# Kernel optimization log

Measured on AMD Instinct MI355X. Metric: run time of the kernel, lower is better.

## Reference

```python
import jax, jax.numpy as jnp
import numpy as np

FG_THRESH = 0.5

def _descriptors(fmap, scribbles):
    # fmap: [B, C, h, w]; scribbles: [B, I, H, W]
    B, C, h, w = fmap.shape
    I = scribbles.shape[1]
    # bilinear resize (align_corners=False == half-pixel, no antialias, like torch)
    sr = jax.image.resize(scribbles, (B, I, h, w), method='bilinear', antialias=False)
    mask = (sr > FG_THRESH).astype(fmap.dtype)                 # [B, I, h, w]
    cnt = mask.sum(axis=(-1, -2))                              # [B, I]
    ssum = jnp.einsum('bihw,bchw->bic', mask, fmap)            # masked sum over HW
    mean = ssum / jnp.maximum(cnt, 1.0)[..., None]             # [B, I, C]
    # fallback when a mask has no foreground pixels: feature at argmax of soft mask
    idx = jnp.argmax(sr.reshape(B, I, h * w), axis=-1)         # [B, I]
    fflat = fmap.reshape(B, C, h * w)
    fb = jnp.take_along_axis(fflat, idx[:, None, :], axis=2)   # [B, C, I]
    fb = fb.transpose(0, 2, 1)                                 # [B, I, C]
    return jnp.where((cnt > 0)[..., None], mean, fb)

def setup_inputs() -> dict:
    key = jax.random.key(0)
    k0, k1, k2, k3 = jax.random.split(key, 4)
    return {
        'feat0': jax.random.normal(k0, (8, 256, 128, 128), dtype=jnp.float32),
        'feat1': jax.random.normal(k1, (8, 256, 64, 64), dtype=jnp.float32),
        'feat2': jax.random.normal(k2, (8, 256, 32, 32), dtype=jnp.float32),
        'scribbles': jax.random.uniform(k3, (8, 16, 512, 512), dtype=jnp.float32),
    }

def reference(feat0, feat1, feat2, scribbles):
    # multi_scale=True, random_bg_queries=False: per-level masked mean pool,
    # then average descriptors across feature levels. Output: [B, I, C]
    d0 = _descriptors(feat0, scribbles)
    d1 = _descriptors(feat1, scribbles)
    d2 = _descriptors(feat2, scribbles)
    return (d0 + d1 + d2) / 3.0
```

## Files before the change

kernel.cpp:

```cpp
#include <hip/hip_runtime.h>
#include <stdint.h>

#define NB 8
#define NI 16
#define NC 256
#define SH 512
#define NCH 84

typedef __bf16 bf16x8 __attribute__((ext_vector_type(8)));
typedef float f32x4 __attribute__((ext_vector_type(4)));
typedef uint32_t u32x4 __attribute__((ext_vector_type(4)));

static const size_t OFF_SSUM = 0;
static const size_t OFF_CNT  = OFF_SSUM + (size_t)3 * NB * NI * NC * 4;
static const size_t OFF_KEY  = OFF_CNT + (size_t)3 * NB * NI * 4;
static const size_t WS_NEED  = OFF_KEY + (size_t)3 * NB * NI * 8;
static const int    ZERO_N4  = (int)(WS_NEED / 16);

__device__ __forceinline__ float4 ld4(const float* p) {
    return *reinterpret_cast<const float4*>(p);
}

__global__ __launch_bounds__(256) void zero_kernel(float4* __restrict__ ws4) {
    const int i = blockIdx.x * 256 + threadIdx.x;
    if (i < ZERO_N4) ws4[i] = make_float4(0.f, 0.f, 0.f, 0.f);
}

__device__ __forceinline__ void mfma_step1(const uint16_t* __restrict__ lmp, int ks, int cl,
                                           const float4 (&buf)[2], f32x4& a0) {
    const uint4 wA = *reinterpret_cast<const uint4*>(lmp + ks * 32);
    u32x4 au;
    au.x = ((wA.x >> cl) & 0x10001u) * 0x3F80u;
    au.y = ((wA.y >> cl) & 0x10001u) * 0x3F80u;
    au.z = ((wA.z >> cl) & 0x10001u) * 0x3F80u;
    au.w = ((wA.w >> cl) & 0x10001u) * 0x3F80u;
    const bf16x8 av = __builtin_bit_cast(bf16x8, au);
    bf16x8 bv;
    bv[0] = (__bf16)buf[0].x; bv[1] = (__bf16)buf[0].y;
    bv[2] = (__bf16)buf[0].z; bv[3] = (__bf16)buf[0].w;
    bv[4] = (__bf16)buf[1].x; bv[5] = (__bf16)buf[1].y;
    bv[6] = (__bf16)buf[1].z; bv[7] = (__bf16)buf[1].w;
    a0 = __builtin_amdgcn_mfma_f32_16x16x32_bf16(av, bv, a0, 0, 0, 0);
}

template<int W, int S, int P>
__device__ __forceinline__ void do_chunk(const float* __restrict__ f,
                                         const float* __restrict__ scr,
                                         float* __restrict__ ssum_lb,
                                         int* __restrict__ cnt_lb,
                                         unsigned long long* __restrict__ key_lb,
                                         int b, int chunk, int tid,
                                         uint8_t* __restrict__ lmask8,
                                         uint16_t* __restrict__ lmask16,
                                         int* __restrict__ lcnt,
                                         unsigned long long* __restrict__ lkey) {
    const int wave = tid >> 6;
    const int lane = tid & 63;
    const int kg = lane >> 4;
    const int cl = lane & 15;
    const int c0 = wave * 16;
    const int kb = chunk * 256;
    const float* fp0 = f + ((size_t)b * NC + c0 + cl) * P + kb + kg * 8;
    float4 buf[4][2];
    #pragma unroll
    for (int k = 0; k < 2; ++k) {
        buf[k][0] = ld4(fp0 + k * 32);
        buf[k][1] = ld4(fp0 + k * 32 + 4);
    }

    const int gi = tid >> 8;
    const int p = tid & 255;
    const int pix = chunk * 256 + p;
    const int y = pix / W;
    const int x = pix - y * W;
    const int r0 = S * y + (S / 2 - 1);
    const int c0s = S * x + (S / 2 - 1);
    const float* sb = scr + ((size_t)b * NI + gi * 4) * (SH * SH) + (size_t)r0 * SH;
    float s4v[4];
    if constexpr (S == 4) {
        float4 q0[4], q1[4];
        #pragma unroll
        for (int i = 0; i < 4; ++i) {
            const float* sp = sb + (size_t)i * (SH * SH);
            q0[i] = ld4(sp + (c0s - 1));
            q1[i] = ld4(sp + SH + (c0s - 1));
        }
        #pragma unroll
        for (int i = 0; i < 4; ++i)
            s4v[i] = (q0[i].y + q0[i].z) + (q1[i].y + q1[i].z);
    } else {
        float qa[4], qb[4], qc[4], qd[4];
        #pragma unroll
        for (int i = 0; i < 4; ++i) {
            const float* sp = sb + (size_t)i * (SH * SH);
            qa[i] = sp[c0s];
            qb[i] = sp[c0s + 1];
            qc[i] = sp[SH + c0s];
            qd[i] = sp[SH + c0s + 1];
        }
        #pragma unroll
        for (int i = 0; i < 4; ++i)
            s4v[i] = (qa[i] + qb[i]) + (qc[i] + qd[i]);
    }
    unsigned int mword = 0;
    #pragma unroll
    for (int i = 0; i < 4; ++i) {
        const float s4 = s4v[i];
        bool bit = s4 > 2.0f;
        mword |= bit ? (1u << i) : 0u;
        unsigned long long bal = __ballot(bit);
        if (lane == 0) atomicAdd(&lcnt[gi * 4 + i], (int)__popcll(bal));
        if (bal == 0ull) {
            unsigned int srb = __float_as_uint(0.25f * s4);
            unsigned int mx = srb;
            #pragma unroll
            for (int off = 1; off < 64; off <<= 1) {
                unsigned int o = __shfl_xor(mx, off, 64);
                mx = (o > mx) ? o : mx;
            }
            unsigned long long win = __ballot(srb == mx);
            if (lane == 0) {
                int wl = __ffsll((unsigned long long)win) - 1;
                unsigned int wpix = (unsigned int)(chunk * 256 + (p & ~63) + wl);
                unsigned long long key = (((unsigned long long)mx) << 32)
                                       | (unsigned long long)(0xFFFFFFFFu - wpix);
                atomicMax(&lkey[gi * 4 + i], key);
            }
        }
    }
    lmask8[gi * 256 + p] = (uint8_t)mword;
    __syncthreads();
    if (tid < 256)
        lmask16[tid] = (uint16_t)((unsigned)lmask8[tid]
                                | ((unsigned)lmask8[256 + tid] << 4)
                                | ((unsigned)lmask8[512 + tid] << 8)
                                | ((unsigned)lmask8[768 + tid] << 12));
    __syncthreads();

    #pragma unroll
    for (int k = 2; k < 4; ++k) {
        buf[k][0] = ld4(fp0 + k * 32);
        buf[k][1] = ld4(fp0 + k * 32 + 4);
    }
    const uint16_t* lmp = lmask16 + kg * 8;
    f32x4 acc = {0.f, 0.f, 0.f, 0.f};
    #pragma unroll
    for (int ks = 0; ks < 8; ++ks) {
        mfma_step1(lmp, ks, cl, buf[ks & 3], acc);
        if (ks + 4 < 8) {
            buf[ks & 3][0] = ld4(fp0 + (ks + 4) * 32);
            buf[ks & 3][1] = ld4(fp0 + (ks + 4) * 32 + 4);
        }
    }
    const int c = c0 + cl;
    #pragma unroll
    for (int r = 0; r < 4; ++r)
        atomicAdd(&ssum_lb[(kg * 4 + r) * NC + c], acc[r]);

    if (tid < NI) {
        int v = lcnt[tid];
        if (v) atomicAdd(&cnt_lb[tid], v);
        unsigned long long k = lkey[tid];
        if (k) atomicMax(&key_lb[tid], k);
    }
}

__global__ __launch_bounds__(1024, 8) void fused_kernel(const float* __restrict__ f0,
                                                        const float* __restrict__ f1,
                                                        const float* __restrict__ f2,
                                                        const float* __restrict__ scr,
                                                        float* __restrict__ ssum,
                                                        int* __restrict__ cnt,
                                                        unsigned long long* __restrict__ key) {
    __shared__ uint8_t lmask8[1024];
    __shared__ __align__(16) uint16_t lmask16[256];
    __shared__ int lcnt[NI];
    __shared__ unsigned long long lkey[NI];
    const int tid = threadIdx.x;
    const int b = blockIdx.y;
    const int bx = blockIdx.x;
    if (tid < NI) { lcnt[tid] = 0; lkey[tid] = 0ull; }
    __syncthreads();
    if (bx < 64) {
        const size_t o = (size_t)(0 * NB + b);
        do_chunk<128, 4, 16384>(f0, scr, ssum + o * NI * NC, cnt + o * NI, key + o * NI,
                                b, bx, tid, lmask8, lmask16, lcnt, lkey);
    } else if (bx < 80) {
        const size_t o = (size_t)(1 * NB + b);
        do_chunk<64, 8, 4096>(f1, scr, ssum + o * NI * NC, cnt + o * NI, key + o * NI,
                              b, bx - 64, tid, lmask8, lmask16, lcnt, lkey);
    } else {
        const size_t o = (size_t)(2 * NB + b);
        do_chunk<32, 16, 1024>(f2, scr, ssum + o * NI * NC, cnt + o * NI, key + o * NI,
                               b, bx - 80, tid, lmask8, lmask16, lcnt, lkey);
    }
}

__global__ __launch_bounds__(256) void final_kernel(const float* __restrict__ f0,
                                                    const float* __restrict__ f1,
                                                    const float* __restrict__ f2,
                                                    const int* __restrict__ cnt,
                                                    const unsigned long long* __restrict__ key,
                                                    const float* __restrict__ ssum,
                                                    float* __restrict__ out) {
    const int bi = blockIdx.x;
    const int c = threadIdx.x;
    const int b = bi >> 4;
    const float* fl[3] = {f0, f1, f2};
    const int Ps[3] = {16384, 4096, 1024};
    float r = 0.f;
    #pragma unroll
    for (int l = 0; l < 3; ++l) {
        const int cn = cnt[l * NB * NI + bi];
        float v;
        if (cn > 0) {
            v = ssum[((size_t)l * NB * NI + bi) * NC + c] / (float)cn;
        } else {
            unsigned int p = 0xFFFFFFFFu -
                (unsigned int)(key[l * NB * NI + bi] & 0xFFFFFFFFull);
            v = fl[l][((size_t)b * NC + c) * Ps[l] + p];
        }
        r += v;
    }
    out[(size_t)bi * NC + c] = r * (1.f / 3.f);
}

extern "C" void kernel_launch(void* const* d_in, const int* in_sizes, int n_in,
                              void* d_out, int out_size, void* d_ws, size_t ws_size,
                              hipStream_t stream) {
    const float* f0  = (const float*)d_in[0];
    const float* f1  = (const float*)d_in[1];
    const float* f2  = (const float*)d_in[2];
    const float* scr = (const float*)d_in[3];
    float* out = (float*)d_out;
    char* ws = (char*)d_ws;
    if (ws_size < WS_NEED) return;

    float* ssum = (float*)(ws + OFF_SSUM);
    int* cnt = (int*)(ws + OFF_CNT);
    unsigned long long* key = (unsigned long long*)(ws + OFF_KEY);

    zero_kernel<<<(ZERO_N4 + 255) / 256, 256, 0, stream>>>((float4*)ws);
    fused_kernel<<<dim3(NCH, NB), 1024, 0, stream>>>(f0, f1, f2, scr, ssum, cnt, key);
    final_kernel<<<NB * NI, NC, 0, stream>>>(f0, f1, f2, cnt, key, ssum, out);
}
```

Baseline: 61.61 us.

## Stage feature tiles through swizzled LDS with coalesced loads for MFMA

Features are now loaded with fully coalesced float4 reads into a 64KB XOR-swizzled shared-memory buffer, one 64-channel slab at a time, instead of each lane reading strided rows directly. The MFMA loop reads its B operand from LDS, and each wave covers a K-half across four channel slabs, so there are four accumulators. The next slab is prefetched into registers while the current one is consumed. Scribble loads are split into two halves to reduce register pressure. The 64KB LDS and the extra barriers per slab limit occupancy and add sync overhead.

```diff
diff --git a/kernel.cpp b/kernel.cpp
--- a/kernel.cpp
+++ b/kernel.cpp
@@ -24,23 +24,6 @@
 __global__ __launch_bounds__(256) void zero_kernel(float4* __restrict__ ws4) {
     const int i = blockIdx.x * 256 + threadIdx.x;
     if (i < ZERO_N4) ws4[i] = make_float4(0.f, 0.f, 0.f, 0.f);
-}
-
-__device__ __forceinline__ void mfma_step1(const uint16_t* __restrict__ lmp, int ks, int cl,
-                                           const float4 (&buf)[2], f32x4& a0) {
-    const uint4 wA = *reinterpret_cast<const uint4*>(lmp + ks * 32);
-    u32x4 au;
-    au.x = ((wA.x >> cl) & 0x10001u) * 0x3F80u;
-    au.y = ((wA.y >> cl) & 0x10001u) * 0x3F80u;
-    au.z = ((wA.z >> cl) & 0x10001u) * 0x3F80u;
-    au.w = ((wA.w >> cl) & 0x10001u) * 0x3F80u;
-    const bf16x8 av = __builtin_bit_cast(bf16x8, au);
-    bf16x8 bv;
-    bv[0] = (__bf16)buf[0].x; bv[1] = (__bf16)buf[0].y;
-    bv[2] = (__bf16)buf[0].z; bv[3] = (__bf16)buf[0].w;
-    bv[4] = (__bf16)buf[1].x; bv[5] = (__bf16)buf[1].y;
-    bv[6] = (__bf16)buf[1].z; bv[7] = (__bf16)buf[1].w;
-    a0 = __builtin_amdgcn_mfma_f32_16x16x32_bf16(av, bv, a0, 0, 0, 0);
 }
 
 template<int W, int S, int P>
@@ -52,21 +35,28 @@
                                          int b, int chunk, int tid,
                                          uint8_t* __restrict__ lmask8,
                                          uint16_t* __restrict__ lmask16,
+                                         char* __restrict__ fbuf,
                                          int* __restrict__ lcnt,
                                          unsigned long long* __restrict__ lkey) {
     const int wave = tid >> 6;
     const int lane = tid & 63;
     const int kg = lane >> 4;
     const int cl = lane & 15;
-    const int c0 = wave * 16;
     const int kb = chunk * 256;
-    const float* fp0 = f + ((size_t)b * NC + c0 + cl) * P + kb + kg * 8;
-    float4 buf[4][2];
-    #pragma unroll
-    for (int k = 0; k < 2; ++k) {
-        buf[k][0] = ld4(fp0 + k * 32);
-        buf[k][1] = ld4(fp0 + k * 32 + 4);
-    }
+    const float* fbase = f + (size_t)b * NC * P + kb;
+
+    int s_rc[4], s_g[4];
+    #pragma unroll
+    for (int s = 0; s < 4; ++s) {
+        const int n = s * 1024 + tid;
+        s_rc[s] = n >> 6;
+        s_g[s] = n & 63;
+    }
+
+    float4 st[4];
+    #pragma unroll
+    for (int s = 0; s < 4; ++s)
+        st[s] = ld4(fbase + (size_t)s_rc[s] * P + s_g[s] * 4);
 
     const int gi = tid >> 8;
     const int p = tid & 255;
@@ -76,55 +66,52 @@
     const int r0 = S * y + (S / 2 - 1);
     const int c0s = S * x + (S / 2 - 1);
     const float* sb = scr + ((size_t)b * NI + gi * 4) * (SH * SH) + (size_t)r0 * SH;
-    float s4v[4];
-    if constexpr (S == 4) {
-        float4 q0[4], q1[4];
+    unsigned int mword = 0;
+    #pragma unroll
+    for (int ii = 0; ii < 4; ii += 2) {
+        float s4v[2];
+        if constexpr (S == 4) {
+            float4 q0[2], q1[2];
+            #pragma unroll
+            for (int j = 0; j < 2; ++j) {
+                const float* sp = sb + (size_t)(ii + j) * (SH * SH);
+                q0[j] = ld4(sp + (c0s - 1));
+                q1[j] = ld4(sp + SH + (c0s - 1));
+            }
+            #pragma unroll
+            for (int j = 0; j < 2; ++j)
+                s4v[j] = (q0[j].y + q0[j].z) + (q1[j].y + q1[j].z);
+        } else {
+            #pragma unroll
+            for (int j = 0; j < 2; ++j) {
+                const float* sp = sb + (size_t)(ii + j) * (SH * SH);
+                s4v[j] = (sp[c0s] + sp[c0s + 1]) + (sp[SH + c0s] + sp[SH + c0s + 1]);
+            }
+        }
         #pragma unroll
-        for (int i = 0; i < 4; ++i) {
-            const float* sp = sb + (size_t)i * (SH * SH);
-            q0[i] = ld4(sp + (c0s - 1));
-            q1[i] = ld4(sp + SH + (c0s - 1));
-        }
-        #pragma unroll
-        for (int i = 0; i < 4; ++i)
-            s4v[i] = (q0[i].y + q0[i].z) + (q1[i].y + q1[i].z);
-    } else {
-        float qa[4], qb[4], qc[4], qd[4];
-        #pragma unroll
-        for (int i = 0; i < 4; ++i) {
-            const float* sp = sb + (size_t)i * (SH * SH);
-            qa[i] = sp[c0s];
-            qb[i] = sp[c0s + 1];
-            qc[i] = sp[SH + c0s];
-            qd[i] = sp[SH + c0s + 1];
-        }
-        #pragma unroll
-        for (int i = 0; i < 4; ++i)
-            s4v[i] = (qa[i] + qb[i]) + (qc[i] + qd[i]);
-    }
-    unsigned int mword = 0;
-    #pragma unroll
-    for (int i = 0; i < 4; ++i) {
-        const float s4 = s4v[i];
-        bool bit = s4 > 2.0f;
-        mword |= bit ? (1u << i) : 0u;
-        unsigned long long bal = __ballot(bit);
-        if (lane == 0) atomicAdd(&lcnt[gi * 4 + i], (int)__popcll(bal));
-        if (bal == 0ull) {
-            unsigned int srb = __float_as_uint(0.25f * s4);
-            unsigned int mx = srb;
-            #pragma unroll
-            for (int off = 1; off < 64; off <<= 1) {
-                unsigned int o = __shfl_xor(mx, off, 64);
-                mx = (o > mx) ? o : mx;
-            }
-            unsigned long long win = __ballot(srb == mx);
-            if (lane == 0) {
-                int wl = __ffsll((unsigned long long)win) - 1;
-                unsigned int wpix = (unsigned int)(chunk * 256 + (p & ~63) + wl);
-                unsigned long long key = (((unsigned long long)mx) << 32)
-                                       | (unsigned long long)(0xFFFFFFFFu - wpix);
-                atomicMax(&lkey[gi * 4 + i], key);
+        for (int j = 0; j < 2; ++j) {
+            const int i = ii + j;
+            const float s4 = s4v[j];
+            bool bit = s4 > 2.0f;
+            mword |= bit ? (1u << i) : 0u;
+            unsigned long long bal = __ballot(bit);
+            if (lane == 0) atomicAdd(&lcnt[gi * 4 + i], (int)__popcll(bal));
+            if (bal == 0ull) {
+                unsigned int srb = __float_as_uint(0.25f * s4);
+                unsigned int mx = srb;
+                #pragma unroll
+                for (int off = 1; off < 64; off <<= 1) {
+                    unsigned int o = __shfl_xor(mx, off, 64);
+                    mx = (o > mx) ? o : mx;
+                }
+                unsigned long long win = __ballot(srb == mx);
+                if (lane == 0) {
+                    int wl = __ffsll((unsigned long long)win) - 1;
+                    unsigned int wpix = (unsigned int)(chunk * 256 + (p & ~63) + wl);
+                    unsigned long long key = (((unsigned long long)mx) << 32)
+                                           | (unsigned long long)(0xFFFFFFFFu - wpix);
+                    atomicMax(&lkey[gi * 4 + i], key);
+                }
             }
         }
     }
@@ -135,28 +122,64 @@
                                 | ((unsigned)lmask8[256 + tid] << 4)
                                 | ((unsigned)lmask8[512 + tid] << 8)
                                 | ((unsigned)lmask8[768 + tid] << 12));
+    #pragma unroll
+    for (int s = 0; s < 4; ++s)
+        *reinterpret_cast<float4*>(fbuf + s_rc[s] * 1024
+                                   + ((s_g[s] ^ (s_rc[s] & 15)) * 16)) = st[s];
     __syncthreads();
 
-    #pragma unroll
-    for (int k = 2; k < 4; ++k) {
-        buf[k][0] = ld4(fp0 + k * 32);
-        buf[k][1] = ld4(fp0 + k * 32 + 4);
-    }
-    const uint16_t* lmp = lmask16 + kg * 8;
-    f32x4 acc = {0.f, 0.f, 0.f, 0.f};
-    #pragma unroll
-    for (int ks = 0; ks < 8; ++ks) {
-        mfma_step1(lmp, ks, cl, buf[ks & 3], acc);
-        if (ks + 4 < 8) {
-            buf[ks & 3][0] = ld4(fp0 + (ks + 4) * 32);
-            buf[ks & 3][1] = ld4(fp0 + (ks + 4) * 32 + 4);
-        }
-    }
-    const int c = c0 + cl;
-    #pragma unroll
-    for (int r = 0; r < 4; ++r)
-        atomicAdd(&ssum_lb[(kg * 4 + r) * NC + c], acc[r]);
-
+    const int ntl = wave & 3;
+    const int kh = wave >> 2;
+    const int rc_r = ntl * 16 + cl;
+    const char* rbase = fbuf + rc_r * 1024;
+    f32x4 acc[4];
+    #pragma unroll
+    for (int q = 0; q < 4; ++q) acc[q] = f32x4{0.f, 0.f, 0.f, 0.f};
+    #pragma unroll
+    for (int qc = 0; qc < 4; ++qc) {
+        if (qc < 3) {
+            #pragma unroll
+            for (int s = 0; s < 4; ++s)
+                st[s] = ld4(fbase + (size_t)((qc + 1) * 64 + s_rc[s]) * P + s_g[s] * 4);
+        }
+        #pragma unroll
+        for (int ks = 0; ks < 2; ++ks) {
+            const int kglob = kh * 2 + ks;
+            const int px = kglob * 32 + kg * 8;
+            const uint4 wA = *reinterpret_cast<const uint4*>(lmask16 + px);
+            u32x4 au;
+            au.x = ((wA.x >> cl) & 0x10001u) * 0x3F80u;
+            au.y = ((wA.y >> cl) & 0x10001u) * 0x3F80u;
+            au.z = ((wA.z >> cl) & 0x10001u) * 0x3F80u;
+            au.w = ((wA.w >> cl) & 0x10001u) * 0x3F80u;
+            const bf16x8 av = __builtin_bit_cast(bf16x8, au);
+            const int g0 = kglob * 8 + kg * 2;
+            float4 v0 = *reinterpret_cast<const float4*>(rbase + ((g0 ^ cl) * 16));
+            float4 v1 = *reinterpret_cast<const float4*>(rbase + (((g0 + 1) ^ cl) * 16));
+            bf16x8 bv;
+            bv[0] = (__bf16)v0.x; bv[1] = (__bf16)v0.y;
+            bv[2] = (__bf16)v0.z; bv[3] = (__bf16)v0.w;
+            bv[4] = (__bf16)v1.x; bv[5] = (__bf16)v1.y;
+            bv[6] = (__bf16)v1.z; bv[7] = (__bf16)v1.w;
+            acc[qc] = __builtin_amdgcn_mfma_f32_16x16x32_bf16(av, bv, acc[qc], 0, 0, 0);
+        }
+        __syncthreads();
+        if (qc < 3) {
+            #pragma unroll
+            for (int s = 0; s < 4; ++s)
+                *reinterpret_cast<float4*>(fbuf + s_rc[s] * 1024
+                                           + ((s_g[s] ^ (s_rc[s] & 15)) * 16)) = st[s];
+            __syncthreads();
+        }
+    }
+
+    #pragma unroll
+    for (int qc = 0; qc < 4; ++qc) {
+        const int c = qc * 64 + ntl * 16 + cl;
+        #pragma unroll
+        for (int r = 0; r < 4; ++r)
+            atomicAdd(&ssum_lb[(kg * 4 + r) * NC + c], acc[qc][r]);
+    }
     if (tid < NI) {
         int v = lcnt[tid];
         if (v) atomicAdd(&cnt_lb[tid], v);
@@ -172,6 +195,7 @@
                                                         float* __restrict__ ssum,
                                                         int* __restrict__ cnt,
                                                         unsigned long long* __restrict__ key) {
+    __shared__ __align__(16) char fbuf[64 * 1024];
     __shared__ uint8_t lmask8[1024];
     __shared__ __align__(16) uint16_t lmask16[256];
     __shared__ int lcnt[NI];
@@ -184,15 +208,15 @@
     if (bx < 64) {
         const size_t o = (size_t)(0 * NB + b);
         do_chunk<128, 4, 16384>(f0, scr, ssum + o * NI * NC, cnt + o * NI, key + o * NI,
-                                b, bx, tid, lmask8, lmask16, lcnt, lkey);
+                                b, bx, tid, lmask8, lmask16, fbuf, lcnt, lkey);
     } else if (bx < 80) {
         const size_t o = (size_t)(1 * NB + b);
         do_chunk<64, 8, 4096>(f1, scr, ssum + o * NI * NC, cnt + o * NI, key + o * NI,
-                              b, bx - 64, tid, lmask8, lmask16, lcnt, lkey);
+                              b, bx - 64, tid, lmask8, lmask16, fbuf, lcnt, lkey);
     } else {
         const size_t o = (size_t)(2 * NB + b);
         do_chunk<32, 16, 1024>(f2, scr, ssum + o * NI * NC, cnt + o * NI, key + o * NI,
-                               b, bx - 80, tid, lmask8, lmask16, lcnt, lkey);
+                               b, bx - 80, tid, lmask8, lmask16, fbuf, lcnt, lkey);
     }
 }
 
```

Result: slower. 79.44 us (+28.9%).
